# Kernel optimization log

Measured on AMD Instinct MI355X. Metric: run time of the kernel, lower is better.

Reference implementation:

```python
import jax, jax.numpy as jnp
import numpy as np

MARGIN = 0.1
CURVATURE = 1.0
EPS = 1e-5  # keep norms strictly inside the Poincare ball for arctanh
B, D = 8192, 256


def setup_inputs() -> dict:
    key = jax.random.key(0)
    k1, k2, k3 = jax.random.split(key, 3)
    # random directions with random radii in (0, 1): valid Poincare-ball points
    v = jax.random.normal(k1, (B, D), dtype=jnp.float32)
    nrm = jnp.linalg.norm(v, axis=-1, keepdims=True)
    r = jax.random.uniform(k2, (B, 1), minval=0.05, maxval=0.95, dtype=jnp.float32)
    embeddings = v / nrm * r
    # precomputed lattice comparison matrix: cmp[i,j] in {-1, 0, 1}
    # (-1: set_i < set_j, 1: set_i > set_j, 0: incomparable). Only i<j is used.
    cmp = jax.random.randint(k3, (B, B), 0, 3, dtype=jnp.int32) - 1
    return {"embeddings": embeddings, "cmp": cmp}


def reference(embeddings, cmp):
    sc = jnp.sqrt(jnp.asarray(CURVATURE, embeddings.dtype))
    # hyperbolic distance from origin: d(x, 0) = (2/sqrt(c)) * artanh(sqrt(c)*||x||)
    nrm = jnp.linalg.norm(embeddings, axis=-1)                      # [B]
    nrm = jnp.clip(nrm, 0.0, (1.0 - EPS) / sc)
    d = (2.0 / sc) * jnp.arctanh(sc * nrm)                          # [B]

    diff = d[:, None] - d[None, :]                                   # [B,B] d_i - d_j
    triu = jnp.triu(jnp.ones((B, B), dtype=bool), k=1)               # pairs i<j only
    m_lt = triu & (cmp == -1)   # ms_i < ms_j: relu(d_i - d_j + margin)
    m_gt = triu & (cmp == 1)    # ms_i > ms_j: relu(d_j - d_i + margin)

    total = (jnp.sum(jnp.where(m_lt, jax.nn.relu(diff + MARGIN), 0.0))
             + jnp.sum(jnp.where(m_gt, jax.nn.relu(-diff + MARGIN), 0.0)))
    n_pairs = jnp.sum(m_lt) + jnp.sum(m_gt)
    return jnp.where(n_pairs > 0, total / n_pairs.astype(embeddings.dtype), 0.0)
```

## Files before the change

### kernel.cpp

```cpp
#include <hip/hip_runtime.h>

constexpr int Bdim = 8192;
constexpr int Ddim = 256;
constexpr int TS   = 512;
constexpr int NTt  = Bdim / TS;
constexpr int NTRI = NTt * (NTt + 1) / 2;
constexpr int RPU  = 16;
constexpr int CPT  = TS / RPU;
constexpr int NUNIT = NTRI * CPT;
constexpr int NBLK  = 2048;
constexpr int RPW   = RPU / 4;
constexpr float MARGIN_F = 0.1f;

typedef int iv4 __attribute__((ext_vector_type(4)));

__global__ __launch_bounds__(256) void k_norm(const float* __restrict__ emb,
                                              float* __restrict__ d) {
    int row  = blockIdx.x * 4 + (threadIdx.x >> 6);
    int lane = threadIdx.x & 63;
    float4 v = ((const float4*)(emb + (size_t)row * Ddim))[lane];
    float s = v.x * v.x + v.y * v.y + v.z * v.z + v.w * v.w;
#pragma unroll
    for (int off = 32; off > 0; off >>= 1) s += __shfl_down(s, off, 64);
    if (lane == 0) {
        float n = fminf(sqrtf(s), 1.0f - 1e-5f);
        d[row] = logf((1.0f + n) / (1.0f - n));
    }
}

#define ACCE(cv, djv, div)                                    \
    {                                                         \
        float x = fmaf((float)(cv), (djv) - (div), MARGIN_F); \
        s += fmaxf(x, 0.0f);                                  \
        cntA += (cv) & 1;                                     \
    }

__global__ __launch_bounds__(256) void k_pairs(const float* __restrict__ d,
                                               const int* __restrict__ cmp,
                                               double* __restrict__ psum,
                                               unsigned int* __restrict__ pcnt) {
    int tid  = threadIdx.x;
    int lane = tid & 63;
    int wave = tid >> 6;

    float s = 0.0f;
    int cntA = 0;
    int cntB = 0;
    int nproc = 0;

    for (int u = blockIdx.x; u < NUNIT; u += NBLK) {
        int tri   = u % NTRI;
        int chunk = u / NTRI;
        int rem = tri, ti = 0;
        while (rem >= NTt - ti) { rem -= NTt - ti; ++ti; }
        int tj = ti + rem;

        int i0 = ti * TS + chunk * RPU + wave * RPW;
        int j0 = tj * TS + lane * 4;
        int j1 = j0 + 256;
        float4 dj0 = *(const float4*)(d + j0);
        float4 dj1 = *(const float4*)(d + j1);
        const iv4* p = (const iv4*)(cmp + (size_t)i0 * Bdim + j0);

        if (ti == tj) {
#pragma unroll
            for (int r = 0; r < RPW; ++r) {
                int   i  = i0 + r;
                float di = d[i];
                const iv4* pr = p + (size_t)r * (Bdim / 4);
                if (j0 + 3 > i) {
                    iv4 c = pr[0];
                    { bool a = (c.x != 0) & (j0 + 0 > i);
                      float x = fmaf((float)c.x, dj0.x - di, MARGIN_F);
                      s += a ? fmaxf(x, 0.0f) : 0.0f; cntB += a ? 1 : 0; }
                    { bool a = (c.y != 0) & (j0 + 1 > i);
                      float x = fmaf((float)c.y, dj0.y - di, MARGIN_F);
                      s += a ? fmaxf(x, 0.0f) : 0.0f; cntB += a ? 1 : 0; }
                    { bool a = (c.z != 0) & (j0 + 2 > i);
                      float x = fmaf((float)c.z, dj0.z - di, MARGIN_F);
                      s += a ? fmaxf(x, 0.0f) : 0.0f; cntB += a ? 1 : 0; }
                    { bool a = (c.w != 0) & (j0 + 3 > i);
                      float x = fmaf((float)c.w, dj0.w - di, MARGIN_F);
                      s += a ? fmaxf(x, 0.0f) : 0.0f; cntB += a ? 1 : 0; }
                }
                if (j1 + 3 > i) {
                    iv4 c = pr[64];
                    { bool a = (c.x != 0) & (j1 + 0 > i);
                      float x = fmaf((float)c.x, dj1.x - di, MARGIN_F);
                      s += a ? fmaxf(x, 0.0f) : 0.0f; cntB += a ? 1 : 0; }
                    { bool a = (c.y != 0) & (j1 + 1 > i);
                      float x = fmaf((float)c.y, dj1.y - di, MARGIN_F);
                      s += a ? fmaxf(x, 0.0f) : 0.0f; cntB += a ? 1 : 0; }
                    { bool a = (c.z != 0) & (j1 + 2 > i);
                      float x = fmaf((float)c.z, dj1.z - di, MARGIN_F);
                      s += a ? fmaxf(x, 0.0f) : 0.0f; cntB += a ? 1 : 0; }
                    { bool a = (c.w != 0) & (j1 + 3 > i);
                      float x = fmaf((float)c.w, dj1.w - di, MARGIN_F);
                      s += a ? fmaxf(x, 0.0f) : 0.0f; cntB += a ? 1 : 0; }
                }
            }
        } else {
            iv4 c0[RPW], c1[RPW];
            float di[RPW];
#pragma unroll
            for (int r = 0; r < RPW; ++r) {
                const iv4* pr = p + (size_t)r * (Bdim / 4);
                c0[r] = pr[0];
                c1[r] = pr[64];
            }
#pragma unroll
            for (int r = 0; r < RPW; ++r) di[r] = d[i0 + r];
#pragma unroll
            for (int r = 0; r < RPW; ++r) {
                ACCE(c0[r].x, dj0.x, di[r]);
                ACCE(c0[r].y, dj0.y, di[r]);
                ACCE(c0[r].z, dj0.z, di[r]);
                ACCE(c0[r].w, dj0.w, di[r]);
                ACCE(c1[r].x, dj1.x, di[r]);
                ACCE(c1[r].y, dj1.y, di[r]);
                ACCE(c1[r].z, dj1.z, di[r]);
                ACCE(c1[r].w, dj1.w, di[r]);
            }
            nproc += 8 * RPW;
        }
    }

    s -= MARGIN_F * (float)(nproc - cntA);
    int cnt = cntA + cntB;

#pragma unroll
    for (int off = 32; off > 0; off >>= 1) {
        s   += __shfl_down(s, off, 64);
        cnt += __shfl_down(cnt, off, 64);
    }
    __shared__ float ws_s[4];
    __shared__ int   ws_c[4];
    if ((tid & 63) == 0) { ws_s[wave] = s; ws_c[wave] = cnt; }
    __syncthreads();
    if (tid == 0) {
        float st = ws_s[0] + ws_s[1] + ws_s[2] + ws_s[3];
        int   ct = ws_c[0] + ws_c[1] + ws_c[2] + ws_c[3];
        psum[blockIdx.x] = (double)st;
        pcnt[blockIdx.x] = (unsigned int)ct;
    }
}

__global__ __launch_bounds__(256) void k_final(const double* __restrict__ psum,
                                               const unsigned int* __restrict__ pcnt,
                                               float* __restrict__ out) {
    int tid = threadIdx.x;
    double s = 0.0;
    unsigned long long c = 0;
    for (int idx = tid; idx < NBLK; idx += 256) {
        s += psum[idx];
        c += pcnt[idx];
    }
#pragma unroll
    for (int off = 32; off > 0; off >>= 1) {
        s += __shfl_down(s, off, 64);
        c += __shfl_down(c, off, 64);
    }
    __shared__ double sd[4];
    __shared__ unsigned long long sc[4];
    int wave = tid >> 6;
    if ((tid & 63) == 0) { sd[wave] = s; sc[wave] = c; }
    __syncthreads();
    if (tid == 0) {
        double st = sd[0] + sd[1] + sd[2] + sd[3];
        unsigned long long ct = sc[0] + sc[1] + sc[2] + sc[3];
        out[0] = (ct > 0) ? (float)(st / (double)ct) : 0.0f;
    }
}

extern "C" void kernel_launch(void* const* d_in, const int* in_sizes, int n_in,
                              void* d_out, int out_size, void* d_ws, size_t ws_size,
                              hipStream_t stream) {
    const float* emb = (const float*)d_in[0];
    const int*   cmp = (const int*)d_in[1];
    float* out = (float*)d_out;

    char* ws = (char*)d_ws;
    float*        dvec = (float*)ws;
    double*       psum = (double*)(ws + 32768);
    unsigned int* pcnt = (unsigned int*)(ws + 32768 + NBLK * 8);

    hipLaunchKernelGGL(k_norm, dim3(Bdim / 4), dim3(256), 0, stream, emb, dvec);
    hipLaunchKernelGGL(k_pairs, dim3(NBLK), dim3(256), 0, stream,
                       dvec, cmp, psum, pcnt);
    hipLaunchKernelGGL(k_final, dim3(1), dim3(256), 0, stream, psum, pcnt, out);
}
```

Before: 35.77 us.

## Fuse final reduction into pair kernel via per-block release flags

```diff
diff --git a/kernel.cpp b/kernel.cpp
--- a/kernel.cpp
+++ b/kernel.cpp
@@ -11,6 +11,7 @@
 constexpr int NBLK  = 2048;
 constexpr int RPW   = RPU / 4;
 constexpr float MARGIN_F = 0.1f;
+constexpr unsigned MAGIC = 0x5EEDC0DEu;
 
 typedef int iv4 __attribute__((ext_vector_type(4)));
 
@@ -28,25 +29,18 @@
     }
 }
 
-#define ACCE(cv, djv, div)                                    \
-    {                                                         \
-        float x = fmaf((float)(cv), (djv) - (div), MARGIN_F); \
-        s += fmaxf(x, 0.0f);                                  \
-        cntA += (cv) & 1;                                     \
-    }
-
 __global__ __launch_bounds__(256) void k_pairs(const float* __restrict__ d,
                                                const int* __restrict__ cmp,
-                                               double* __restrict__ psum,
-                                               unsigned int* __restrict__ pcnt) {
+                                               float* __restrict__ psumf,
+                                               unsigned int* __restrict__ pcntv,
+                                               unsigned int* __restrict__ pflag,
+                                               float* __restrict__ out) {
     int tid  = threadIdx.x;
     int lane = tid & 63;
     int wave = tid >> 6;
 
     float s = 0.0f;
-    int cntA = 0;
-    int cntB = 0;
-    int nproc = 0;
+    int cnt = 0;
 
     for (int u = blockIdx.x; u < NUNIT; u += NBLK) {
         int tri   = u % NTRI;
@@ -72,61 +66,59 @@
                     iv4 c = pr[0];
                     { bool a = (c.x != 0) & (j0 + 0 > i);
                       float x = fmaf((float)c.x, dj0.x - di, MARGIN_F);
-                      s += a ? fmaxf(x, 0.0f) : 0.0f; cntB += a ? 1 : 0; }
+                      s += a ? fmaxf(x, 0.0f) : 0.0f; cnt += a ? 1 : 0; }
                     { bool a = (c.y != 0) & (j0 + 1 > i);
                       float x = fmaf((float)c.y, dj0.y - di, MARGIN_F);
-                      s += a ? fmaxf(x, 0.0f) : 0.0f; cntB += a ? 1 : 0; }
+                      s += a ? fmaxf(x, 0.0f) : 0.0f; cnt += a ? 1 : 0; }
                     { bool a = (c.z != 0) & (j0 + 2 > i);
                       float x = fmaf((float)c.z, dj0.z - di, MARGIN_F);
-                      s += a ? fmaxf(x, 0.0f) : 0.0f; cntB += a ? 1 : 0; }
+                      s += a ? fmaxf(x, 0.0f) : 0.0f; cnt += a ? 1 : 0; }
                     { bool a = (c.w != 0) & (j0 + 3 > i);
                       float x = fmaf((float)c.w, dj0.w - di, MARGIN_F);
-                      s += a ? fmaxf(x, 0.0f) : 0.0f; cntB += a ? 1 : 0; }
+                      s += a ? fmaxf(x, 0.0f) : 0.0f; cnt += a ? 1 : 0; }
                 }
                 if (j1 + 3 > i) {
                     iv4 c = pr[64];
                     { bool a = (c.x != 0) & (j1 + 0 > i);
                       float x = fmaf((float)c.x, dj1.x - di, MARGIN_F);
-                      s += a ? fmaxf(x, 0.0f) : 0.0f; cntB += a ? 1 : 0; }
+                      s += a ? fmaxf(x, 0.0f) : 0.0f; cnt += a ? 1 : 0; }
                     { bool a = (c.y != 0) & (j1 + 1 > i);
                       float x = fmaf((float)c.y, dj1.y - di, MARGIN_F);
-                      s += a ? fmaxf(x, 0.0f) : 0.0f; cntB += a ? 1 : 0; }
+                      s += a ? fmaxf(x, 0.0f) : 0.0f; cnt += a ? 1 : 0; }
                     { bool a = (c.z != 0) & (j1 + 2 > i);
                       float x = fmaf((float)c.z, dj1.z - di, MARGIN_F);
-                      s += a ? fmaxf(x, 0.0f) : 0.0f; cntB += a ? 1 : 0; }
+                      s += a ? fmaxf(x, 0.0f) : 0.0f; cnt += a ? 1 : 0; }
                     { bool a = (c.w != 0) & (j1 + 3 > i);
                       float x = fmaf((float)c.w, dj1.w - di, MARGIN_F);
-                      s += a ? fmaxf(x, 0.0f) : 0.0f; cntB += a ? 1 : 0; }
+                      s += a ? fmaxf(x, 0.0f) : 0.0f; cnt += a ? 1 : 0; }
                 }
             }
         } else {
-            iv4 c0[RPW], c1[RPW];
-            float di[RPW];
 #pragma unroll
             for (int r = 0; r < RPW; ++r) {
+                float di = d[i0 + r];
                 const iv4* pr = p + (size_t)r * (Bdim / 4);
-                c0[r] = pr[0];
-                c1[r] = pr[64];
+                iv4 c0 = pr[0];
+                iv4 c1 = pr[64];
+                { bool a = c0.x != 0; float x = fmaf((float)c0.x, dj0.x - di, MARGIN_F);
+                  s += a ? fmaxf(x, 0.0f) : 0.0f; cnt += a ? 1 : 0; }
+                { bool a = c0.y != 0; float x = fmaf((float)c0.y, dj0.y - di, MARGIN_F);
+                  s += a ? fmaxf(x, 0.0f) : 0.0f; cnt += a ? 1 : 0; }
+                { bool a = c0.z != 0; float x = fmaf((float)c0.z, dj0.z - di, MARGIN_F);
+                  s += a ? fmaxf(x, 0.0f) : 0.0f; cnt += a ? 1 : 0; }
+                { bool a = c0.w != 0; float x = fmaf((float)c0.w, dj0.w - di, MARGIN_F);
+                  s += a ? fmaxf(x, 0.0f) : 0.0f; cnt += a ? 1 : 0; }
+                { bool a = c1.x != 0; float x = fmaf((float)c1.x, dj1.x - di, MARGIN_F);
+                  s += a ? fmaxf(x, 0.0f) : 0.0f; cnt += a ? 1 : 0; }
+                { bool a = c1.y != 0; float x = fmaf((float)c1.y, dj1.y - di, MARGIN_F);
+                  s += a ? fmaxf(x, 0.0f) : 0.0f; cnt += a ? 1 : 0; }
+                { bool a = c1.z != 0; float x = fmaf((float)c1.z, dj1.z - di, MARGIN_F);
+                  s += a ? fmaxf(x, 0.0f) : 0.0f; cnt += a ? 1 : 0; }
+                { bool a = c1.w != 0; float x = fmaf((float)c1.w, dj1.w - di, MARGIN_F);
+                  s += a ? fmaxf(x, 0.0f) : 0.0f; cnt += a ? 1 : 0; }
             }
-#pragma unroll
-            for (int r = 0; r < RPW; ++r) di[r] = d[i0 + r];
-#pragma unroll
-            for (int r = 0; r < RPW; ++r) {
-                ACCE(c0[r].x, dj0.x, di[r]);
-                ACCE(c0[r].y, dj0.y, di[r]);
-                ACCE(c0[r].z, dj0.z, di[r]);
-                ACCE(c0[r].w, dj0.w, di[r]);
-                ACCE(c1[r].x, dj1.x, di[r]);
-                ACCE(c1[r].y, dj1.y, di[r]);
-                ACCE(c1[r].z, dj1.z, di[r]);
-                ACCE(c1[r].w, dj1.w, di[r]);
-            }
-            nproc += 8 * RPW;
         }
     }
-
-    s -= MARGIN_F * (float)(nproc - cntA);
-    int cnt = cntA + cntB;
 
 #pragma unroll
     for (int off = 32; off > 0; off >>= 1) {
@@ -140,35 +132,43 @@
     if (tid == 0) {
         float st = ws_s[0] + ws_s[1] + ws_s[2] + ws_s[3];
         int   ct = ws_c[0] + ws_c[1] + ws_c[2] + ws_c[3];
-        psum[blockIdx.x] = (double)st;
-        pcnt[blockIdx.x] = (unsigned int)ct;
+        int b = blockIdx.x;
+        __hip_atomic_store(&psumf[b], st, __ATOMIC_RELAXED,
+                           __HIP_MEMORY_SCOPE_AGENT);
+        __hip_atomic_store(&pcntv[b], (unsigned)ct, __ATOMIC_RELAXED,
+                           __HIP_MEMORY_SCOPE_AGENT);
+        __hip_atomic_store(&pflag[b], MAGIC ^ (unsigned)b, __ATOMIC_RELEASE,
+                           __HIP_MEMORY_SCOPE_AGENT);
     }
-}
 
-__global__ __launch_bounds__(256) void k_final(const double* __restrict__ psum,
-                                               const unsigned int* __restrict__ pcnt,
-                                               float* __restrict__ out) {
-    int tid = threadIdx.x;
-    double s = 0.0;
-    unsigned long long c = 0;
-    for (int idx = tid; idx < NBLK; idx += 256) {
-        s += psum[idx];
-        c += pcnt[idx];
-    }
+    if (blockIdx.x == NBLK - 1) {
+        double sd_ = 0.0;
+        unsigned long long cc = 0;
+        for (int idx = tid; idx < NBLK; idx += 256) {
+            while (__hip_atomic_load(&pflag[idx], __ATOMIC_ACQUIRE,
+                                     __HIP_MEMORY_SCOPE_AGENT)
+                   != (MAGIC ^ (unsigned)idx)) {
+                __builtin_amdgcn_s_sleep(8);
+            }
+            sd_ += (double)__hip_atomic_load(&psumf[idx], __ATOMIC_RELAXED,
+                                             __HIP_MEMORY_SCOPE_AGENT);
+            cc  += __hip_atomic_load(&pcntv[idx], __ATOMIC_RELAXED,
+                                     __HIP_MEMORY_SCOPE_AGENT);
+        }
 #pragma unroll
-    for (int off = 32; off > 0; off >>= 1) {
-        s += __shfl_down(s, off, 64);
-        c += __shfl_down(c, off, 64);
-    }
-    __shared__ double sd[4];
-    __shared__ unsigned long long sc[4];
-    int wave = tid >> 6;
-    if ((tid & 63) == 0) { sd[wave] = s; sc[wave] = c; }
-    __syncthreads();
-    if (tid == 0) {
-        double st = sd[0] + sd[1] + sd[2] + sd[3];
-        unsigned long long ct = sc[0] + sc[1] + sc[2] + sc[3];
-        out[0] = (ct > 0) ? (float)(st / (double)ct) : 0.0f;
+        for (int off = 32; off > 0; off >>= 1) {
+            sd_ += __shfl_down(sd_, off, 64);
+            cc  += __shfl_down(cc, off, 64);
+        }
+        __shared__ double rd[4];
+        __shared__ unsigned long long rc[4];
+        if ((tid & 63) == 0) { rd[wave] = sd_; rc[wave] = cc; }
+        __syncthreads();
+        if (tid == 0) {
+            double st = rd[0] + rd[1] + rd[2] + rd[3];
+            unsigned long long ct = rc[0] + rc[1] + rc[2] + rc[3];
+            out[0] = (ct > 0) ? (float)(st / (double)ct) : 0.0f;
+        }
     }
 }
 
@@ -180,12 +180,12 @@
     float* out = (float*)d_out;
 
     char* ws = (char*)d_ws;
-    float*        dvec = (float*)ws;
-    double*       psum = (double*)(ws + 32768);
-    unsigned int* pcnt = (unsigned int*)(ws + 32768 + NBLK * 8);
+    float*        dvec  = (float*)ws;
+    float*        psumf = (float*)(ws + 32768);
+    unsigned int* pcntv = (unsigned int*)(ws + 40960);
+    unsigned int* pflag = (unsigned int*)(ws + 49152);
 
     hipLaunchKernelGGL(k_norm, dim3(Bdim / 4), dim3(256), 0, stream, emb, dvec);
     hipLaunchKernelGGL(k_pairs, dim3(NBLK), dim3(256), 0, stream,
-                       dvec, cmp, psum, pcnt);
-    hipLaunchKernelGGL(k_final, dim3(1), dim3(256), 0, stream, psum, pcnt, out);
+                       dvec, cmp, psumf, pcntv, pflag, out);
 }
```

Result: slower. 84.27 us (+135.6%).
